# Kernel tuning notes

Hardware: AMD Instinct MI355X
Metric: run time of the kernel (lower is better)

## Reference

```python
import jax, jax.numpy as jnp
import numpy as np

HSPACES = [1024, 1024, 1024, 1024]   # hypothesis-space sizes
C = 3                                 # num_of_classifiers
EPSILON = 10                          # max rejection-sampling attempts
BATCH = 8192
# tensor_split at cumulative boundaries -> item counts per policy split
ITEM_COUNTS = [HSPACES[0] + HSPACES[1]] + list(HSPACES[2:])  # [2048, 1024, 1024]
HALL = sum(HSPACES)  # 4096


def setup_inputs() -> dict:
    key = jax.random.key(0)
    kx, kw, kb = jax.random.split(key, 3)
    X = jax.random.normal(kx, (BATCH, HALL * C), dtype=jnp.float32)
    W = jax.random.normal(kw, (len(ITEM_COUNTS), C), dtype=jnp.float32) * 0.1
    b = jax.random.normal(kb, (len(ITEM_COUNTS),), dtype=jnp.float32) * 0.1
    return {"X": X, "W": W, "b": b}


def _scores(X, W, b):
    # per-split Linear(3,1) + softmax over items, then concat -> (B, HALL)
    parts = []
    start = 0
    for d, n in enumerate(ITEM_COUNTS):
        obs = X[:, start:start + n * C].reshape(-1, n, C)          # (B, n, 3)
        logits = jnp.einsum('bnc,c->bn', obs, W[d]) + b[d]          # (B, n)
        parts.append(jax.nn.softmax(logits, axis=1))
        start += n * C
    return jnp.concatenate(parts, axis=1)                           # (B, HALL)


def reference(X, W, b):
    scores = _scores(X, W, b)                                       # (B, HALL) probs
    logp = jnp.log(scores)
    key = jax.random.key(42)
    B = scores.shape[0]
    # vectorized epsilon rejection sampling: draw EPSILON samples per row;
    # take `best` if any draw hits it (loop breaks there), else the last draw
    samples = jax.random.categorical(key, logp, shape=(EPSILON, B))  # (EPS, B)
    best = jnp.argmax(scores, axis=1)                                # (B,)
    hit = (samples == best[None, :]).any(axis=0)                     # (B,)
    actions = jnp.where(hit, best, samples[-1])
    return actions
```

## Files before the change

kernel.cpp:

```cpp
#include <hip/hip_runtime.h>
#include <stdint.h>

#define BATCH   8192
#define HALL    4096
#define TPB     256
#define PERT    16
#define EPS     10
#define BH      33554432u

__device__ __forceinline__ uint32_t rotl32(uint32_t x, int r) {
    return __builtin_amdgcn_alignbit(x, x, 32 - r);
}

__device__ __forceinline__ uint32_t threefry_bits_k42(uint32_t lo) {
    const uint32_t ks0 = 0u;
    const uint32_t ks1 = 42u;
    const uint32_t ks2 = 0x1BD11BDAu ^ 42u;
    uint32_t x0 = 0u + ks0;
    uint32_t x1 = lo + ks1;
#define TF_R(r) { x0 += x1; x1 = rotl32(x1, r); x1 ^= x0; }
    TF_R(13) TF_R(15) TF_R(26) TF_R(6)   x0 += ks1; x1 += ks2 + 1u;
    TF_R(17) TF_R(29) TF_R(16) TF_R(24)  x0 += ks2; x1 += ks0 + 2u;
    TF_R(13) TF_R(15) TF_R(26) TF_R(6)   x0 += ks0; x1 += ks1 + 3u;
    TF_R(17) TF_R(29) TF_R(16) TF_R(24)  x0 += ks1; x1 += ks2 + 4u;
    TF_R(13) TF_R(15) TF_R(26) TF_R(6)   x0 += ks2; x1 += ks0 + 5u;
#undef TF_R
    return x0 ^ x1;
}

__global__ __launch_bounds__(TPB, 2)
void reinforce_kernel(const float* __restrict__ X, const float* __restrict__ W,
                      const float* __restrict__ bias, int* __restrict__ out) {
#pragma clang fp contract(off)
    __shared__ float s_ip[HALL];
    __shared__ float s_rm[3][4];
    __shared__ float s_rs[3][4];
    __shared__ float s_rv[EPS + 1][4];
    __shared__ int   s_ri[EPS + 1][4];

    const int b   = blockIdx.x;
    const int tid = threadIdx.x;
    const int wv  = tid >> 6;
    const int ln  = tid & 63;
    const float* xr = X + (size_t)b * (HALL * 3);

    const float w00 = W[0], w01 = W[1], w02 = W[2], bb0 = bias[0];
    const float w10 = W[3], w11 = W[4], w12 = W[5], bb1 = bias[1];
    const float w20 = W[6], w21 = W[7], w22 = W[8], bb2 = bias[2];

    float lg[PERT];
#pragma unroll
    for (int j = 0; j < PERT; j++) {
        int h = tid + j * TPB;
        float x0 = xr[3 * h], x1 = xr[3 * h + 1], x2 = xr[3 * h + 2];
        float wa, wb, wc, bb;
        if (j < 8)       { wa = w00; wb = w01; wc = w02; bb = bb0; }
        else if (j < 12) { wa = w10; wb = w11; wc = w12; bb = bb1; }
        else             { wa = w20; wb = w21; wc = w22; bb = bb2; }
        lg[j] = ((x0 * wa + x1 * wb) + x2 * wc) + bb;
    }

    float pm0 = -INFINITY, pm1 = -INFINITY, pm2 = -INFINITY;
#pragma unroll
    for (int j = 0; j < PERT; j++) {
        if (j < 8)       pm0 = fmaxf(pm0, lg[j]);
        else if (j < 12) pm1 = fmaxf(pm1, lg[j]);
        else             pm2 = fmaxf(pm2, lg[j]);
    }
    for (int off = 32; off; off >>= 1) {
        pm0 = fmaxf(pm0, __shfl_down(pm0, off, 64));
        pm1 = fmaxf(pm1, __shfl_down(pm1, off, 64));
        pm2 = fmaxf(pm2, __shfl_down(pm2, off, 64));
    }
    if (ln == 0) { s_rm[0][wv] = pm0; s_rm[1][wv] = pm1; s_rm[2][wv] = pm2; }
    __syncthreads();
    const float m0 = fmaxf(fmaxf(s_rm[0][0], s_rm[0][1]), fmaxf(s_rm[0][2], s_rm[0][3]));
    const float m1 = fmaxf(fmaxf(s_rm[1][0], s_rm[1][1]), fmaxf(s_rm[1][2], s_rm[1][3]));
    const float m2 = fmaxf(fmaxf(s_rm[2][0], s_rm[2][1]), fmaxf(s_rm[2][2], s_rm[2][3]));

    float ex[PERT];
    float ps0 = 0.f, ps1 = 0.f, ps2 = 0.f;
#pragma unroll
    for (int j = 0; j < PERT; j++) {
        float m = (j < 8) ? m0 : (j < 12) ? m1 : m2;
        float e = expf(lg[j] - m);
        ex[j] = e;
        if (j < 8)       ps0 += e;
        else if (j < 12) ps1 += e;
        else             ps2 += e;
    }
    for (int off = 32; off; off >>= 1) {
        ps0 += __shfl_down(ps0, off, 64);
        ps1 += __shfl_down(ps1, off, 64);
        ps2 += __shfl_down(ps2, off, 64);
    }
    if (ln == 0) { s_rs[0][wv] = ps0; s_rs[1][wv] = ps1; s_rs[2][wv] = ps2; }
    __syncthreads();
    const float s0 = ((s_rs[0][0] + s_rs[0][1]) + s_rs[0][2]) + s_rs[0][3];
    const float s1 = ((s_rs[1][0] + s_rs[1][1]) + s_rs[1][2]) + s_rs[1][3];
    const float s2 = ((s_rs[2][0] + s_rs[2][1]) + s_rs[2][2]) + s_rs[2][3];

    const float is0 = 1.0f / s0, is1 = 1.0f / s1, is2 = 1.0f / s2;
    float bv = -INFINITY; int bi = 0;
#pragma unroll
    for (int j = 0; j < PERT; j++) {
        float sS  = (j < 8) ? s0  : (j < 12) ? s1  : s2;
        float isS = (j < 8) ? is0 : (j < 12) ? is1 : is2;
        float pt = ex[j] * isS;
        int h = tid + j * TPB;
        if (pt > bv) { bv = pt; bi = h; }
        s_ip[h] = sS / ex[j];
    }

    float qmv[EPS]; int qix[EPS];
#pragma unroll
    for (int e = 0; e < EPS; e++) { qmv[e] = INFINITY; qix[e] = 0x7fffffff; }

    const uint32_t rowbase = (uint32_t)b * (uint32_t)HALL;
#pragma unroll 1
    for (int j = 0; j < PERT; j++) {
        int h = tid + j * TPB;
        float ipj = s_ip[h];
        uint32_t cnt = rowbase + (uint32_t)h;
#pragma unroll
        for (int e = 0; e < EPS; e++) {
            uint32_t bits = threefry_bits_k42(cnt + (uint32_t)e * BH);
            uint32_t fb = __builtin_amdgcn_alignbit(0x7Fu, bits, 9);
            float f = __uint_as_float(fb) - 1.0f;
            float a = -__log2f(f);
            float q = a * ipj;
            if (q < qmv[e]) { qmv[e] = q; qix[e] = h; }
        }
    }

#pragma unroll
    for (int e = 0; e < EPS; e++) {
        float q = qmv[e];
        int   i = qix[e];
        for (int off = 32; off; off >>= 1) {
            float qv = __shfl_down(q, off, 64);
            int   ri = __shfl_down(i, off, 64);
            if (qv < q || (qv == q && ri < i)) { q = qv; i = ri; }
        }
        if (ln == 0) { s_rv[e][wv] = q; s_ri[e][wv] = i; }
    }
    {
        float r = bv; int i = bi;
        for (int off = 32; off; off >>= 1) {
            float rv = __shfl_down(r, off, 64);
            int   ri = __shfl_down(i, off, 64);
            if (rv > r || (rv == r && ri < i)) { r = rv; i = ri; }
        }
        if (ln == 0) { s_rv[EPS][wv] = r; s_ri[EPS][wv] = i; }
    }
    __syncthreads();

    if (tid == 0) {
        int samp[EPS];
#pragma unroll
        for (int e = 0; e < EPS; e++) {
            float q = s_rv[e][0]; int i = s_ri[e][0];
#pragma unroll
            for (int w = 1; w < 4; w++) {
                float qv = s_rv[e][w]; int ri = s_ri[e][w];
                if (qv < q || (qv == q && ri < i)) { q = qv; i = ri; }
            }
            samp[e] = i;
        }
        float r = s_rv[EPS][0]; int best = s_ri[EPS][0];
#pragma unroll
        for (int w = 1; w < 4; w++) {
            float rv = s_rv[EPS][w]; int ri = s_ri[EPS][w];
            if (rv > r || (rv == r && ri < best)) { r = rv; best = ri; }
        }
        bool hit = false;
#pragma unroll
        for (int k = 0; k < EPS; k++) hit = hit || (samp[k] == best);
        out[b] = hit ? best : samp[EPS - 1];
    }
}

extern "C" void kernel_launch(void* const* d_in, const int* in_sizes, int n_in,
                              void* d_out, int out_size, void* d_ws, size_t ws_size,
                              hipStream_t stream) {
    const float* X    = (const float*)d_in[0];
    const float* W    = (const float*)d_in[1];
    const float* bias = (const float*)d_in[2];
    int* out = (int*)d_out;
    (void)in_sizes; (void)n_in; (void)d_ws; (void)ws_size; (void)out_size;

    reinforce_kernel<<<BATCH, TPB, 0, stream>>>(X, W, bias, out);
}
```

Measured before the change: 1.026 ms.

## Restructure sampling loop to interleave four Threefry streams per epsilon

Loop order changes so the outer loop runs over the EPS draws and the inner loop over item chunks. Four independent Threefry hash chains are computed together to expose instruction-level parallelism, and per-draw state shrinks from ten min/index pairs to one max/index pair. The keyed constants are folded inline, and the -log minimization is rewritten as maximization of log2(u)*ip. This trades register pressure for ILP, and the wave reduction now runs inside the e-loop.

```diff
diff --git a/kernel.cpp b/kernel.cpp
--- a/kernel.cpp
+++ b/kernel.cpp
@@ -7,26 +7,16 @@
 #define PERT    16
 #define EPS     10
 #define BH      33554432u
+#define NCH     4
 
 __device__ __forceinline__ uint32_t rotl32(uint32_t x, int r) {
     return __builtin_amdgcn_alignbit(x, x, 32 - r);
 }
 
-__device__ __forceinline__ uint32_t threefry_bits_k42(uint32_t lo) {
-    const uint32_t ks0 = 0u;
-    const uint32_t ks1 = 42u;
-    const uint32_t ks2 = 0x1BD11BDAu ^ 42u;
-    uint32_t x0 = 0u + ks0;
-    uint32_t x1 = lo + ks1;
-#define TF_R(r) { x0 += x1; x1 = rotl32(x1, r); x1 ^= x0; }
-    TF_R(13) TF_R(15) TF_R(26) TF_R(6)   x0 += ks1; x1 += ks2 + 1u;
-    TF_R(17) TF_R(29) TF_R(16) TF_R(24)  x0 += ks2; x1 += ks0 + 2u;
-    TF_R(13) TF_R(15) TF_R(26) TF_R(6)   x0 += ks0; x1 += ks1 + 3u;
-    TF_R(17) TF_R(29) TF_R(16) TF_R(24)  x0 += ks1; x1 += ks2 + 4u;
-    TF_R(13) TF_R(15) TF_R(26) TF_R(6)   x0 += ks2; x1 += ks0 + 5u;
-#undef TF_R
-    return x0 ^ x1;
-}
+#define TF_R4(r)  { _Pragma("unroll") for (int k = 0; k < NCH; k++) { \
+                      x0[k] += x1[k]; x1[k] = rotl32(x1[k], (r)); x1[k] ^= x0[k]; } }
+#define TF_I4(ca, cb) { _Pragma("unroll") for (int k = 0; k < NCH; k++) { \
+                      x0[k] += (ca); x1[k] += (cb); } }
 
 __global__ __launch_bounds__(TPB, 2)
 void reinforce_kernel(const float* __restrict__ X, const float* __restrict__ W,
@@ -112,38 +102,49 @@
         s_ip[h] = sS / ex[j];
     }
 
-    float qmv[EPS]; int qix[EPS];
+    const uint32_t tb = (uint32_t)b * (uint32_t)HALL + (uint32_t)tid;
+    const uint32_t ks2p = 0x1BD11BDAu ^ 42u;
+
+#pragma unroll 1
+    for (int e = 0; e < EPS; e++) {
+        const uint32_t eoff = ((uint32_t)e << 25) + 42u;
+        float tmax = -INFINITY; int imax = 0x7fffffff;
+
+#pragma unroll 1
+        for (int jj = 0; jj < PERT; jj += NCH) {
+            uint32_t x0[NCH], x1[NCH];
+            float ip[NCH];
 #pragma unroll
-    for (int e = 0; e < EPS; e++) { qmv[e] = INFINITY; qix[e] = 0x7fffffff; }
+            for (int k = 0; k < NCH; k++) {
+                int h = tid + (jj + k) * TPB;
+                ip[k] = s_ip[h];
+                x0[k] = 0u;
+                x1[k] = tb + (uint32_t)((jj + k) * TPB) + eoff;
+            }
+            TF_R4(13) TF_R4(15) TF_R4(26) TF_R4(6)   TF_I4(42u,  ks2p + 1u)
+            TF_R4(17) TF_R4(29) TF_R4(16) TF_R4(24)  TF_I4(ks2p, 2u)
+            TF_R4(13) TF_R4(15) TF_R4(26) TF_R4(6)   TF_I4(0u,   42u + 3u)
+            TF_R4(17) TF_R4(29) TF_R4(16) TF_R4(24)  TF_I4(42u,  ks2p + 4u)
+            TF_R4(13) TF_R4(15) TF_R4(26) TF_R4(6)   TF_I4(ks2p, 5u)
+#pragma unroll
+            for (int k = 0; k < NCH; k++) {
+                uint32_t bits = x0[k] ^ x1[k];
+                uint32_t fb = __builtin_amdgcn_alignbit(0x7Fu, bits, 9);
+                float f = __uint_as_float(fb) - 1.0f;
+                float t = __log2f(f) * ip[k];
+                int h = tid + (jj + k) * TPB;
+                if (t > tmax) { tmax = t; imax = h; }
+            }
+        }
 
-    const uint32_t rowbase = (uint32_t)b * (uint32_t)HALL;
-#pragma unroll 1
-    for (int j = 0; j < PERT; j++) {
-        int h = tid + j * TPB;
-        float ipj = s_ip[h];
-        uint32_t cnt = rowbase + (uint32_t)h;
-#pragma unroll
-        for (int e = 0; e < EPS; e++) {
-            uint32_t bits = threefry_bits_k42(cnt + (uint32_t)e * BH);
-            uint32_t fb = __builtin_amdgcn_alignbit(0x7Fu, bits, 9);
-            float f = __uint_as_float(fb) - 1.0f;
-            float a = -__log2f(f);
-            float q = a * ipj;
-            if (q < qmv[e]) { qmv[e] = q; qix[e] = h; }
+        for (int off = 32; off; off >>= 1) {
+            float tv = __shfl_down(tmax, off, 64);
+            int   ti = __shfl_down(imax, off, 64);
+            if (tv > tmax || (tv == tmax && ti < imax)) { tmax = tv; imax = ti; }
         }
+        if (ln == 0) { s_rv[e][wv] = tmax; s_ri[e][wv] = imax; }
     }
 
-#pragma unroll
-    for (int e = 0; e < EPS; e++) {
-        float q = qmv[e];
-        int   i = qix[e];
-        for (int off = 32; off; off >>= 1) {
-            float qv = __shfl_down(q, off, 64);
-            int   ri = __shfl_down(i, off, 64);
-            if (qv < q || (qv == q && ri < i)) { q = qv; i = ri; }
-        }
-        if (ln == 0) { s_rv[e][wv] = q; s_ri[e][wv] = i; }
-    }
     {
         float r = bv; int i = bi;
         for (int off = 32; off; off >>= 1) {
@@ -159,11 +160,11 @@
         int samp[EPS];
 #pragma unroll
         for (int e = 0; e < EPS; e++) {
-            float q = s_rv[e][0]; int i = s_ri[e][0];
+            float t = s_rv[e][0]; int i = s_ri[e][0];
 #pragma unroll
             for (int w = 1; w < 4; w++) {
-                float qv = s_rv[e][w]; int ri = s_ri[e][w];
-                if (qv < q || (qv == q && ri < i)) { q = qv; i = ri; }
+                float tv = s_rv[e][w]; int ri = s_ri[e][w];
+                if (tv > t || (tv == t && ri < i)) { t = tv; i = ri; }
             }
             samp[e] = i;
         }
```

Result: slower. 1.227 ms (+19.7%).

## Assign contiguous 16-item chunks per thread with vectorized loads and register-held probabilities

Applied to the files above, without the earlier changes.

Each thread now owns 16 contiguous hypotheses, so its 48 input floats are read as twelve float4 loads instead of strided scalar loads. Each wave falls entirely inside one softmax split, so the three-way reductions become one reduction per wave. The inverse probabilities stay in registers instead of a 16 KB shared array, which together with raising the launch-bounds occupancy hint to 8 blocks allows more resident blocks. The sampling loop is fully unrolled and rewritten as a max over log2(u)*ip, which carries more register pressure and relies on the tie-break order still matching the reference.

```diff
diff --git a/kernel.cpp b/kernel.cpp
--- a/kernel.cpp
+++ b/kernel.cpp
@@ -6,7 +6,6 @@
 #define TPB     256
 #define PERT    16
 #define EPS     10
-#define BH      33554432u
 
 __device__ __forceinline__ uint32_t rotl32(uint32_t x, int r) {
     return __builtin_amdgcn_alignbit(x, x, 32 - r);
@@ -28,13 +27,12 @@
     return x0 ^ x1;
 }
 
-__global__ __launch_bounds__(TPB, 2)
+__global__ __launch_bounds__(TPB, 8)
 void reinforce_kernel(const float* __restrict__ X, const float* __restrict__ W,
                       const float* __restrict__ bias, int* __restrict__ out) {
 #pragma clang fp contract(off)
-    __shared__ float s_ip[HALL];
-    __shared__ float s_rm[3][4];
-    __shared__ float s_rs[3][4];
+    __shared__ float s_rm[4];
+    __shared__ float s_rs[4];
     __shared__ float s_rv[EPS + 1][4];
     __shared__ int   s_ri[EPS + 1][4];
 
@@ -42,110 +40,84 @@
     const int tid = threadIdx.x;
     const int wv  = tid >> 6;
     const int ln  = tid & 63;
-    const float* xr = X + (size_t)b * (HALL * 3);
+    const int sp  = (wv < 2) ? 0 : (wv - 1);
 
-    const float w00 = W[0], w01 = W[1], w02 = W[2], bb0 = bias[0];
-    const float w10 = W[3], w11 = W[4], w12 = W[5], bb1 = bias[1];
-    const float w20 = W[6], w21 = W[7], w22 = W[8], bb2 = bias[2];
+    const float wa = W[3 * sp + 0], wb = W[3 * sp + 1], wc = W[3 * sp + 2];
+    const float bb = bias[sp];
 
+    const float4* x4 = (const float4*)(X + (size_t)b * (HALL * 3)) + (size_t)tid * 12;
     float lg[PERT];
 #pragma unroll
-    for (int j = 0; j < PERT; j++) {
-        int h = tid + j * TPB;
-        float x0 = xr[3 * h], x1 = xr[3 * h + 1], x2 = xr[3 * h + 2];
-        float wa, wb, wc, bb;
-        if (j < 8)       { wa = w00; wb = w01; wc = w02; bb = bb0; }
-        else if (j < 12) { wa = w10; wb = w11; wc = w12; bb = bb1; }
-        else             { wa = w20; wb = w21; wc = w22; bb = bb2; }
-        lg[j] = ((x0 * wa + x1 * wb) + x2 * wc) + bb;
+    for (int c = 0; c < 4; c++) {
+        float4 a0 = x4[3 * c + 0];
+        float4 a1 = x4[3 * c + 1];
+        float4 a2 = x4[3 * c + 2];
+        lg[4 * c + 0] = ((a0.x * wa + a0.y * wb) + a0.z * wc) + bb;
+        lg[4 * c + 1] = ((a0.w * wa + a1.x * wb) + a1.y * wc) + bb;
+        lg[4 * c + 2] = ((a1.z * wa + a1.w * wb) + a2.x * wc) + bb;
+        lg[4 * c + 3] = ((a2.y * wa + a2.z * wb) + a2.w * wc) + bb;
     }
 
-    float pm0 = -INFINITY, pm1 = -INFINITY, pm2 = -INFINITY;
+    float pm = lg[0];
 #pragma unroll
-    for (int j = 0; j < PERT; j++) {
-        if (j < 8)       pm0 = fmaxf(pm0, lg[j]);
-        else if (j < 12) pm1 = fmaxf(pm1, lg[j]);
-        else             pm2 = fmaxf(pm2, lg[j]);
-    }
-    for (int off = 32; off; off >>= 1) {
-        pm0 = fmaxf(pm0, __shfl_down(pm0, off, 64));
-        pm1 = fmaxf(pm1, __shfl_down(pm1, off, 64));
-        pm2 = fmaxf(pm2, __shfl_down(pm2, off, 64));
-    }
-    if (ln == 0) { s_rm[0][wv] = pm0; s_rm[1][wv] = pm1; s_rm[2][wv] = pm2; }
+    for (int k = 1; k < PERT; k++) pm = fmaxf(pm, lg[k]);
+    for (int off = 32; off; off >>= 1) pm = fmaxf(pm, __shfl_down(pm, off, 64));
+    if (ln == 0) s_rm[wv] = pm;
     __syncthreads();
-    const float m0 = fmaxf(fmaxf(s_rm[0][0], s_rm[0][1]), fmaxf(s_rm[0][2], s_rm[0][3]));
-    const float m1 = fmaxf(fmaxf(s_rm[1][0], s_rm[1][1]), fmaxf(s_rm[1][2], s_rm[1][3]));
-    const float m2 = fmaxf(fmaxf(s_rm[2][0], s_rm[2][1]), fmaxf(s_rm[2][2], s_rm[2][3]));
+    const float m = (wv < 2) ? fmaxf(s_rm[0], s_rm[1]) : s_rm[wv];
 
     float ex[PERT];
-    float ps0 = 0.f, ps1 = 0.f, ps2 = 0.f;
+    float ps = 0.f;
 #pragma unroll
-    for (int j = 0; j < PERT; j++) {
-        float m = (j < 8) ? m0 : (j < 12) ? m1 : m2;
-        float e = expf(lg[j] - m);
-        ex[j] = e;
-        if (j < 8)       ps0 += e;
-        else if (j < 12) ps1 += e;
-        else             ps2 += e;
-    }
-    for (int off = 32; off; off >>= 1) {
-        ps0 += __shfl_down(ps0, off, 64);
-        ps1 += __shfl_down(ps1, off, 64);
-        ps2 += __shfl_down(ps2, off, 64);
-    }
-    if (ln == 0) { s_rs[0][wv] = ps0; s_rs[1][wv] = ps1; s_rs[2][wv] = ps2; }
+    for (int k = 0; k < PERT; k++) { float e = expf(lg[k] - m); ex[k] = e; ps += e; }
+    for (int off = 32; off; off >>= 1) ps += __shfl_down(ps, off, 64);
+    if (ln == 0) s_rs[wv] = ps;
     __syncthreads();
-    const float s0 = ((s_rs[0][0] + s_rs[0][1]) + s_rs[0][2]) + s_rs[0][3];
-    const float s1 = ((s_rs[1][0] + s_rs[1][1]) + s_rs[1][2]) + s_rs[1][3];
-    const float s2 = ((s_rs[2][0] + s_rs[2][1]) + s_rs[2][2]) + s_rs[2][3];
+    const float s = (wv < 2) ? (s_rs[0] + s_rs[1]) : s_rs[wv];
 
-    const float is0 = 1.0f / s0, is1 = 1.0f / s1, is2 = 1.0f / s2;
-    float bv = -INFINITY; int bi = 0;
+    const float is = 1.0f / s;
+    float ip[PERT];
+    float bv = -INFINITY; int bk = 0;
 #pragma unroll
-    for (int j = 0; j < PERT; j++) {
-        float sS  = (j < 8) ? s0  : (j < 12) ? s1  : s2;
-        float isS = (j < 8) ? is0 : (j < 12) ? is1 : is2;
-        float pt = ex[j] * isS;
-        int h = tid + j * TPB;
-        if (pt > bv) { bv = pt; bi = h; }
-        s_ip[h] = sS / ex[j];
+    for (int k = 0; k < PERT; k++) {
+        float pt = ex[k] * is;
+        if (pt > bv) { bv = pt; bk = k; }
+        ip[k] = s / ex[k];
     }
 
-    float qmv[EPS]; int qix[EPS];
+    const uint32_t tb2 = (uint32_t)b * (uint32_t)HALL + (uint32_t)tid * (uint32_t)PERT;
+    const int hbase = tid * PERT;
+
+    float qmv[EPS]; int qik[EPS];
 #pragma unroll
-    for (int e = 0; e < EPS; e++) { qmv[e] = INFINITY; qix[e] = 0x7fffffff; }
+    for (int e = 0; e < EPS; e++) { qmv[e] = -INFINITY; qik[e] = 0; }
 
-    const uint32_t rowbase = (uint32_t)b * (uint32_t)HALL;
-#pragma unroll 1
-    for (int j = 0; j < PERT; j++) {
-        int h = tid + j * TPB;
-        float ipj = s_ip[h];
-        uint32_t cnt = rowbase + (uint32_t)h;
+#pragma unroll
+    for (int k = 0; k < PERT; k++) {
+        const float ipk = ip[k];
 #pragma unroll
         for (int e = 0; e < EPS; e++) {
-            uint32_t bits = threefry_bits_k42(cnt + (uint32_t)e * BH);
+            uint32_t bits = threefry_bits_k42(tb2 + (uint32_t)(k + (e << 25)));
             uint32_t fb = __builtin_amdgcn_alignbit(0x7Fu, bits, 9);
             float f = __uint_as_float(fb) - 1.0f;
-            float a = -__log2f(f);
-            float q = a * ipj;
-            if (q < qmv[e]) { qmv[e] = q; qix[e] = h; }
+            float t = __log2f(f) * ipk;
+            if (t > qmv[e]) { qmv[e] = t; qik[e] = k; }
         }
     }
 
 #pragma unroll
     for (int e = 0; e < EPS; e++) {
-        float q = qmv[e];
-        int   i = qix[e];
+        float t = qmv[e];
+        int   i = hbase + qik[e];
         for (int off = 32; off; off >>= 1) {
-            float qv = __shfl_down(q, off, 64);
-            int   ri = __shfl_down(i, off, 64);
-            if (qv < q || (qv == q && ri < i)) { q = qv; i = ri; }
+            float tv = __shfl_down(t, off, 64);
+            int   ti = __shfl_down(i, off, 64);
+            if (tv > t || (tv == t && ti < i)) { t = tv; i = ti; }
         }
-        if (ln == 0) { s_rv[e][wv] = q; s_ri[e][wv] = i; }
+        if (ln == 0) { s_rv[e][wv] = t; s_ri[e][wv] = i; }
     }
     {
-        float r = bv; int i = bi;
+        float r = bv; int i = hbase + bk;
         for (int off = 32; off; off >>= 1) {
             float rv = __shfl_down(r, off, 64);
             int   ri = __shfl_down(i, off, 64);
@@ -159,11 +131,11 @@
         int samp[EPS];
 #pragma unroll
         for (int e = 0; e < EPS; e++) {
-            float q = s_rv[e][0]; int i = s_ri[e][0];
+            float t = s_rv[e][0]; int i = s_ri[e][0];
 #pragma unroll
             for (int w = 1; w < 4; w++) {
-                float qv = s_rv[e][w]; int ri = s_ri[e][w];
-                if (qv < q || (qv == q && ri < i)) { q = qv; i = ri; }
+                float tv = s_rv[e][w]; int ri = s_ri[e][w];
+                if (tv > t || (tv == t && ri < i)) { t = tv; i = ri; }
             }
             samp[e] = i;
         }
```

Measured after the change: 1.039 ms. About the same (+1.3%).
